# Performance work log

Hardware: AMD Instinct MI355X
Metric: run time of the kernel (lower is better)

## Reference

```python
import jax, jax.numpy as jnp
import numpy as np

B, S, H, D = 2, 2048, 16, 128
HID = H * D
THETA = 10000.0
SCALE = 1.0 / np.sqrt(D)


def setup_inputs() -> dict:
    key = jax.random.key(0)
    k1, k2, k3 = jax.random.split(key, 3)
    x = jax.random.normal(k1, (B, S, HID), dtype=jnp.float32)
    w_qkv = jax.random.normal(k2, (3 * HID, HID), dtype=jnp.float32) * 0.02
    w_o = jax.random.normal(k3, (HID, HID), dtype=jnp.float32) * 0.02
    return {"x": x, "w_qkv": w_qkv, "w_o": w_o}


def _rope_cos_sin(seq_len, dim, dtype):
    inv_freq = 1.0 / (THETA ** (jnp.arange(0, dim, 2, dtype=jnp.float32) / dim))
    pos = jnp.arange(seq_len, dtype=jnp.float32)
    freqs = pos[:, None] * inv_freq[None, :]          # (S, D/2)
    emb = jnp.concatenate([freqs, freqs], axis=-1)    # (S, D)
    return jnp.cos(emb).astype(dtype), jnp.sin(emb).astype(dtype)


def _rotate_half(t):
    t1, t2 = jnp.split(t, 2, axis=-1)
    return jnp.concatenate([-t2, t1], axis=-1)


def reference(x, w_qkv, w_o):
    b, s, _ = x.shape
    qkv = jnp.einsum('bsh,oh->bso', x, w_qkv)                 # (B,S,3*HID)
    qkv = qkv.reshape(b, s, 3, H, D).transpose(2, 0, 3, 1, 4)  # (3,B,H,S,D)
    q, k, v = qkv[0], qkv[1], qkv[2]
    cos, sin = _rope_cos_sin(s, D, x.dtype)                    # (S,D)
    q = q * cos + _rotate_half(q) * sin
    k = k * cos + _rotate_half(k) * sin
    scores = jnp.einsum('bhqd,bhkd->bhqk', q, k) * SCALE       # (B,H,S,S)
    causal = jnp.triu(jnp.ones((s, s), dtype=bool), k=1)
    scores = jnp.where(causal[None, None], -jnp.inf, scores)
    attn = jax.nn.softmax(scores.astype(jnp.float32), axis=-1).astype(q.dtype)
    out = jnp.einsum('bhqk,bhkd->bhqd', attn, v)               # (B,H,S,D)
    out = out.transpose(0, 2, 1, 3).reshape(b, s, HID)
    return jnp.einsum('bsh,oh->bso', out, w_o)
```

## Files before the change

### kernel.cpp

```cpp
#include <hip/hip_runtime.h>
#include <hip/hip_bf16.h>

typedef unsigned short u16;
typedef unsigned long long u64;
typedef u16 us8 __attribute__((ext_vector_type(8)));
typedef __bf16 bf8_t __attribute__((ext_vector_type(8)));
typedef float f32x4 __attribute__((ext_vector_type(4)));

__device__ __forceinline__ float b2f(u16 u) {
    return __uint_as_float(((unsigned int)u) << 16);
}
__device__ __forceinline__ u16 f2b(float f) {
    union { __hip_bfloat16 h; u16 u; } v;
    v.h = __float2bfloat16(f);
    return v.u;
}
__device__ __forceinline__ f32x4 mfma16(bf8_t a, bf8_t b, f32x4 c) {
    return __builtin_amdgcn_mfma_f32_16x16x32_bf16(a, b, c, 0, 0, 0);
}
__device__ __forceinline__ void gload_lds16(const u16* g, u16* lds_base) {
    __builtin_amdgcn_global_load_lds((const __attribute__((address_space(1))) unsigned int*)g,
                                     (__attribute__((address_space(3))) unsigned int*)lds_base,
                                     16, 0, 0);
}

__global__ __launch_bounds__(256) void f32_to_bf16(const float* __restrict__ src,
                                                   u16* __restrict__ dst, int n8) {
    int idx = blockIdx.x * 256 + threadIdx.x;
    if (idx >= n8) return;
    float4 f0 = ((const float4*)src)[idx * 2];
    float4 f1 = ((const float4*)src)[idx * 2 + 1];
    us8 o;
    o[0] = f2b(f0.x); o[1] = f2b(f0.y); o[2] = f2b(f0.z); o[3] = f2b(f0.w);
    o[4] = f2b(f1.x); o[5] = f2b(f1.y); o[6] = f2b(f1.z); o[7] = f2b(f1.w);
    ((us8*)dst)[idx] = o;
}

#define BARX() __builtin_amdgcn_s_barrier()
#define LGKM0() do { asm volatile("s_waitcnt lgkmcnt(0)" ::: "memory"); \
                     __builtin_amdgcn_sched_barrier(0); } while (0)
#define VMN() do { \
    if constexpr (AH == 2) asm volatile("s_waitcnt vmcnt(4)" ::: "memory"); \
    else                   asm volatile("s_waitcnt vmcnt(2)" ::: "memory"); \
    __builtin_amdgcn_sched_barrier(0); } while (0)

template<int SF32, int AH>
__global__ __launch_bounds__(512, 2) void gemm256(const u16* __restrict__ A,
                                                  const u16* __restrict__ B,
                                                  void* __restrict__ Cout, int ldc) {
    constexpr int MF = AH * 4;
    constexpr int MH = AH * 2;

    __shared__ u16 LA[2][AH * 128 * 64];
    __shared__ u16 LB[2][256 * 64];

    const int tid = threadIdx.x;
    const int w = tid >> 6, lane = tid & 63;
    const int lm = lane & 15, lq = lane >> 4;
    const int wm = w >> 2, wn = w & 3;

    const int bid = blockIdx.x;
    const int nper = gridDim.x >> 3;
    const int wg = (bid & 7) * nper + (bid >> 3);
    const int mt = (AH == 2) ? (wg & 15) : (wg & 31);
    const int nt = (AH == 2) ? (wg >> 4) : (wg >> 5);
    const int m0 = mt * (AH * 128), n0 = nt * 256;

    const int srow = lane >> 3;
    const int scol = ((lane & 7) ^ srow) * 8;

    const u16* Ag = A + (size_t)(m0 + srow) * 2048 + scol;
    const u16* Bg = B + (size_t)(n0 + srow) * 2048 + scol;

#define STAGE_A(c, h, kt) do { \
    _Pragma("unroll") \
    for (int i = 0; i < 2; i++) { \
        int R = w * 2 + i; \
        gload_lds16(Ag + (size_t)((h) * 128 + R * 8) * 2048 + (kt) * 64, \
                    &LA[c][((h) * 128 + R * 8) * 64]); \
    } } while (0)

#define STAGE_B(c, h, kt) do { \
    _Pragma("unroll") \
    for (int i = 0; i < 2; i++) { \
        int R = w * 2 + i; \
        gload_lds16(Bg + (size_t)((h) * 128 + R * 8) * 2048 + (kt) * 64, \
                    &LB[c][((h) * 128 + R * 8) * 64]); \
    } } while (0)

    bf8_t af[MF][2], bfr[4][2];
    f32x4 acc[MF][4] = {};
    const int cswz = (lm & 7) << 4;

#define RD_A(c, mh) do { \
    _Pragma("unroll") \
    for (int m = 0; m < MH; m++) \
    _Pragma("unroll") \
    for (int ks = 0; ks < 2; ks++) { \
        int row = wm * (AH * 64) + ((mh) * MH + m) * 16 + lm; \
        int o = (row * 128 + ks * 64 + lq * 16) ^ cswz; \
        af[(mh) * MH + m][ks] = *(const bf8_t*)((const char*)&LA[c][0] + o); \
    } } while (0)

#define RD_B(c, nh) do { \
    _Pragma("unroll") \
    for (int n = 0; n < 2; n++) \
    _Pragma("unroll") \
    for (int ks = 0; ks < 2; ks++) { \
        int row = wn * 64 + ((nh) * 2 + n) * 16 + lm; \
        int o = (row * 128 + ks * 64 + lq * 16) ^ cswz; \
        bfr[(nh) * 2 + n][ks] = *(const bf8_t*)((const char*)&LB[c][0] + o); \
    } } while (0)

#define QUAD(mh, nh) do { \
    __builtin_amdgcn_s_setprio(1); \
    _Pragma("unroll") \
    for (int m = 0; m < MH; m++) \
    _Pragma("unroll") \
    for (int n = 0; n < 2; n++) \
    _Pragma("unroll") \
    for (int ks = 0; ks < 2; ks++) \
        acc[(mh) * MH + m][(nh) * 2 + n] = mfma16(af[(mh) * MH + m][ks], \
            bfr[(nh) * 2 + n][ks], acc[(mh) * MH + m][(nh) * 2 + n]); \
    __builtin_amdgcn_s_setprio(0); \
    } while (0)

#define TILE(c, tB, tA) do { \
    RD_A(c, 0); RD_B(c, 0); \
    STAGE_B((c) ^ 1, 0, tB); \
    BARX(); LGKM0(); \
    QUAD(0, 0); \
    BARX(); \
    RD_A(c, 1); \
    STAGE_B((c) ^ 1, 1, tB); \
    BARX(); LGKM0(); \
    QUAD(1, 0); \
    BARX(); \
    RD_B(c, 1); \
    STAGE_A(c, 0, tA); \
    BARX(); LGKM0(); \
    QUAD(0, 1); \
    BARX(); \
    if constexpr (AH == 2) STAGE_A(c, 1, tA); \
    QUAD(1, 1); \
    VMN(); \
    BARX(); \
} while (0)

    STAGE_A(0, 0, 0);
    if constexpr (AH == 2) STAGE_A(0, 1, 0);
    STAGE_B(0, 0, 0); STAGE_B(0, 1, 0);
    STAGE_A(1, 0, 1);
    if constexpr (AH == 2) STAGE_A(1, 1, 1);
    VMN();
    BARX();

    for (int it = 0; it < 16; it++) {
        const int t0 = 2 * it, t1 = 2 * it + 1;
        const int tB0 = t1;
        const int tA0 = (t0 + 2 < 32) ? t0 + 2 : 31;
        const int tB1 = (t1 + 1 < 32) ? t1 + 1 : 31;
        const int tA1 = (t1 + 2 < 32) ? t1 + 2 : 31;
        TILE(0, tB0, tA0);
        TILE(1, tB1, tA1);
    }

#pragma unroll
    for (int m = 0; m < MF; m++)
#pragma unroll
        for (int n = 0; n < 4; n++)
#pragma unroll
            for (int r = 0; r < 4; r++) {
                int row = m0 + wm * (AH * 64) + m * 16 + lq * 4 + r;
                int col = n0 + wn * 64 + n * 16 + lm;
                if (SF32)
                    ((float*)Cout)[(size_t)row * ldc + col] = acc[m][n][r];
                else
                    ((u16*)Cout)[(size_t)row * ldc + col] = f2b(acc[m][n][r]);
            }
#undef TILE
#undef QUAD
#undef RD_A
#undef RD_B
#undef STAGE_A
#undef STAGE_B
}

__global__ __launch_bounds__(256) void rope_vt(u16* __restrict__ qkv, u16* __restrict__ VT) {
    __shared__ u16 T[64 * 136];
    const int tid = threadIdx.x;
    const int s0 = blockIdx.x * 64;
    const int bh = blockIdx.y;
    const int b = bh >> 4, h = bh & 15;
#pragma unroll
    for (int p = 0; p < 4; p++) {
        int sl = p * 16 + (tid >> 4);
        int d0 = (tid & 15) * 8;
        *(us8*)&T[sl * 136 + d0] =
            *(const us8*)(qkv + ((size_t)(b * 2048 + s0 + sl)) * 6144 + 4096 + h * 128 + d0);
    }
#pragma unroll
    for (int p = 0; p < 2; p++) {
        int task = p * 256 + tid;
        int sl = task >> 3;
        int jg = task & 7;
        size_t base = ((size_t)(b * 2048 + s0 + sl)) * 6144 + h * 128 + jg * 8;
        us8 qlo = *(const us8*)(qkv + base);
        us8 qhi = *(const us8*)(qkv + base + 64);
        us8 klo = *(const us8*)(qkv + base + 2048);
        us8 khi = *(const us8*)(qkv + base + 2048 + 64);
        us8 oql, oqh, okl, okh;
        float s = (float)(s0 + sl);
#pragma unroll
        for (int e = 0; e < 8; e++) {
            int j = jg * 8 + e;
            float inv = __expf((float)j * (-9.210340371976184f / 64.f));
            float ang = s * inv;
            float sn, c;
            __sincosf(ang, &sn, &c);
            float q1 = b2f(qlo[e]), q2 = b2f(qhi[e]);
            oql[e] = f2b(q1 * c - q2 * sn);
            oqh[e] = f2b(q2 * c + q1 * sn);
            float k1 = b2f(klo[e]), k2 = b2f(khi[e]);
            okl[e] = f2b(k1 * c - k2 * sn);
            okh[e] = f2b(k2 * c + k1 * sn);
        }
        *(us8*)(qkv + base) = oql;
        *(us8*)(qkv + base + 64) = oqh;
        *(us8*)(qkv + base + 2048) = okl;
        *(us8*)(qkv + base + 2048 + 64) = okh;
    }
    __syncthreads();
#pragma unroll
    for (int p = 0; p < 4; p++) {
        int idx = p * 256 + tid;
        int d = idx & 127;
        int sg = idx >> 7;
        us8 v;
#pragma unroll
        for (int i = 0; i < 8; i++) v[i] = T[(sg * 8 + i) * 136 + d];
        *(us8*)&VT[((size_t)bh * 128 + d) * 2048 + s0 + sg * 8] = v;
    }
}

#define ATT_SCALE 0.08838834764831845f

__global__ __launch_bounds__(256, 2) void attn_flash(const u16* __restrict__ qkv, const u16* __restrict__ VT,
                                                     u16* __restrict__ AO) {
    const int bid = blockIdx.x;
    const int swz = (bid & 7) * 64 + (bid >> 3);
    const int bh = swz >> 4;
    const int pair = swz & 15;
    const int b = bh >> 4, h = bh & 15;
    const int tid = threadIdx.x, lane = tid & 63, wave = tid >> 6;
    const int lm = lane & 15, lq = lane >> 4;

    const int jq0 = 31 - pair;
    const int jq1 = pair;
    const int ktmax = jq0;

    __shared__ u16 Kt[64 * 136];
    __shared__ u16 Vt[128 * 72];

    bf8_t qf[2][4];
#pragma unroll
    for (int qg = 0; qg < 2; qg++) {
        const int jqv = qg ? jq1 : jq0;
        const u16* Qrow = qkv + ((size_t)(b * 2048 + jqv * 64 + wave * 16 + lm)) * 6144 + h * 128;
#pragma unroll
        for (int ks = 0; ks < 4; ks++)
            qf[qg][ks] = *(const bf8_t*)(Qrow + ks * 32 + lq * 8);
    }

    f32x4 Of[2][8] = {};
    float mrun[2] = {-3.0e38f, -3.0e38f}, lrun[2] = {0.f, 0.f};

    const u16* Kbase = qkv + (size_t)b * 2048 * 6144 + 2048 + h * 128;
    const u16* VTbase = VT + (size_t)bh * 128 * 2048;

    const int krow = tid >> 4;
    const int kcol = (tid & 15) * 8;
    const int vrow = tid >> 3;
    const int vcol = (tid & 7) * 8;

    us8 kreg[4], vreg[4];
#pragma unroll
    for (int p = 0; p < 4; p++) {
        kreg[p] = *(const us8*)(Kbase + (size_t)(p * 16 + krow) * 6144 + kcol);
        vreg[p] = *(const us8*)(VTbase + (size_t)(p * 32 + vrow) * 2048 + vcol);
    }

    for (int kt = 0; kt <= ktmax; kt++) {
        __syncthreads();
#pragma unroll
        for (int p = 0; p < 4; p++) {
            *(us8*)&Kt[(p * 16 + krow) * 136 + kcol] = kreg[p];
            *(us8*)&Vt[(p * 32 + vrow) * 72 + vcol] = vreg[p];
        }
        __syncthreads();
        {
            int kn = (kt + 1 <= ktmax ? kt + 1 : ktmax) * 64;
#pragma unroll
            for (int p = 0; p < 4; p++) {
                kreg[p] = *(const us8*)(Kbase + (size_t)(kn + p * 16 + krow) * 6144 + kcol);
                vreg[p] = *(const us8*)(VTbase + (size_t)(p * 32 + vrow) * 2048 + kn + vcol);
            }
        }

        const bool act1 = (kt <= jq1);
        u64 pk[2][4];
#pragma unroll
        for (int qg = 0; qg < 2; qg++) {
            if (qg == 0 || act1) {
                const int jqv = qg ? jq1 : jq0;
                float sv[4][4];
#pragma unroll
                for (int nb = 0; nb < 4; nb++) {
                    f32x4 a = {};
#pragma unroll
                    for (int ks = 0; ks < 4; ks++) {
                        bf8_t kf = *(const bf8_t*)&Kt[(nb * 16 + lm) * 136 + ks * 32 + lq * 8];
                        a = mfma16(kf, qf[qg][ks], a);
                    }
#pragma unroll
                    for (int r = 0; r < 4; r++) sv[nb][r] = a[r] * ATT_SCALE;
                }
                if (kt == jqv) {
                    int qglob = jqv * 64 + wave * 16 + lm;
#pragma unroll
                    for (int nb = 0; nb < 4; nb++)
#pragma unroll
                        for (int r = 0; r < 4; r++)
                            if (kt * 64 + nb * 16 + lq * 4 + r > qglob) sv[nb][r] = -3.0e38f;
                }
                float mx = -3.0e38f;
#pragma unroll
                for (int nb = 0; nb < 4; nb++)
#pragma unroll
                    for (int r = 0; r < 4; r++) mx = fmaxf(mx, sv[nb][r]);
                mx = fmaxf(mx, __shfl_xor(mx, 16, 64));
                mx = fmaxf(mx, __shfl_xor(mx, 32, 64));
                float mnew = fmaxf(mrun[qg], mx);
                float a_ = __expf(mrun[qg] - mnew);
                float rs = 0.f;
#pragma unroll
                for (int nb = 0; nb < 4; nb++) {
                    float e0 = __expf(sv[nb][0] - mnew), e1 = __expf(sv[nb][1] - mnew);
                    float e2 = __expf(sv[nb][2] - mnew), e3 = __expf(sv[nb][3] - mnew);
                    rs += (e0 + e1) + (e2 + e3);
                    unsigned int lo = (unsigned int)f2b(e0) | ((unsigned int)f2b(e1) << 16);
                    unsigned int hi = (unsigned int)f2b(e2) | ((unsigned int)f2b(e3) << 16);
                    pk[qg][nb] = (u64)lo | ((u64)hi << 32);
                }
                rs += __shfl_xor(rs, 16, 64);
                rs += __shfl_xor(rs, 32, 64);
                lrun[qg] = lrun[qg] * a_ + rs;
                mrun[qg] = mnew;
#pragma unroll
                for (int db = 0; db < 8; db++)
#pragma unroll
                    for (int r = 0; r < 4; r++) Of[qg][db][r] *= a_;
            }
        }

        const int slo = ((lq & 1) * 2) * 16 + lm;
        const int shi = slo + 16;
        const bool sel = (lq >> 1) != 0;
#pragma unroll
        for (int kk = 0; kk < 2; kk++) {
            union { u64 v[2]; bf8_t f; } pf[2];
#pragma unroll
            for (int qg = 0; qg < 2; qg++) {
                if (qg == 0 || act1) {
                    u64 lo0 = __shfl(pk[qg][2 * kk + 0], slo, 64);
                    u64 lo1 = __shfl(pk[qg][2 * kk + 1], slo, 64);
                    u64 hi0 = __shfl(pk[qg][2 * kk + 0], shi, 64);
                    u64 hi1 = __shfl(pk[qg][2 * kk + 1], shi, 64);
                    pf[qg].v[0] = sel ? lo1 : lo0;
                    pf[qg].v[1] = sel ? hi1 : hi0;
                }
            }
#pragma unroll
            for (int db = 0; db < 8; db++) {
                bf8_t vf = *(const bf8_t*)&Vt[(db * 16 + lm) * 72 + kk * 32 + lq * 8];
                Of[0][db] = mfma16(vf, pf[0].f, Of[0][db]);
                if (act1) Of[1][db] = mfma16(vf, pf[1].f, Of[1][db]);
            }
        }
    }
#pragma unroll
    for (int qg = 0; qg < 2; qg++) {
        const int jqv = qg ? jq1 : jq0;
        float invl = 1.f / lrun[qg];
        size_t rowbase = (size_t)(b * 2048 + jqv * 64 + wave * 16 + lm) * 2048 + h * 128;
#pragma unroll
        for (int db = 0; db < 8; db++) {
            ushort4 o;
            o.x = f2b(Of[qg][db][0] * invl);
            o.y = f2b(Of[qg][db][1] * invl);
            o.z = f2b(Of[qg][db][2] * invl);
            o.w = f2b(Of[qg][db][3] * invl);
            *(ushort4*)(AO + rowbase + db * 16 + lq * 4) = o;
        }
    }
}

extern "C" void kernel_launch(void* const* d_in, const int* in_sizes, int n_in,
                              void* d_out, int out_size, void* d_ws, size_t ws_size,
                              hipStream_t stream) {
    const float* x     = (const float*)d_in[0];
    const float* w_qkv = (const float*)d_in[1];
    const float* w_o   = (const float*)d_in[2];
    float* out = (float*)d_out;
    u16* ws = (u16*)d_ws;

    u16* qkvb  = ws;
    u16* VT    = ws + 25165824;
    u16* AO    = ws + 33554432;
    u16* xb    = ws + 41943040;
    u16* wqkvb = ws + 50331648;
    u16* wob   = ws + 62914560;

    f32_to_bf16<<<4096, 256, 0, stream>>>(x, xb, 1048576);
    f32_to_bf16<<<6144, 256, 0, stream>>>(w_qkv, wqkvb, 1572864);
    f32_to_bf16<<<2048, 256, 0, stream>>>(w_o, wob, 524288);
    gemm256<0, 2><<<384, 512, 0, stream>>>(xb, wqkvb, qkvb, 6144);
    rope_vt<<<dim3(32, 32), 256, 0, stream>>>(qkvb, VT);
    attn_flash<<<dim3(512), 256, 0, stream>>>(qkvb, VT, AO);
    gemm256<1, 1><<<256, 512, 0, stream>>>(AO, wob, out, 2048);
}
```

Measured before the change: 416.1 us.

## Retile QKV GEMM to 256x192 blocks for a single full wave

Replaces the 256x256 QKV projection GEMM with a 256x192 tile kernel so the grid has 512 blocks, matching two blocks per CU across the device instead of a partial second wave. The warp layout and the LDS staging and pipelining schedule are reworked for the new tile shape. The output projection GEMM is split into its own specialized kernel with unchanged logic. The narrower tile lowers per-block reuse and changes the wait-count pipelining, which could expose load latency.

```diff
diff --git a/kernel.cpp b/kernel.cpp
--- a/kernel.cpp
+++ b/kernel.cpp
@@ -39,32 +39,25 @@
 #define BARX() __builtin_amdgcn_s_barrier()
 #define LGKM0() do { asm volatile("s_waitcnt lgkmcnt(0)" ::: "memory"); \
                      __builtin_amdgcn_sched_barrier(0); } while (0)
-#define VMN() do { \
-    if constexpr (AH == 2) asm volatile("s_waitcnt vmcnt(4)" ::: "memory"); \
-    else                   asm volatile("s_waitcnt vmcnt(2)" ::: "memory"); \
-    __builtin_amdgcn_sched_barrier(0); } while (0)
-
-template<int SF32, int AH>
-__global__ __launch_bounds__(512, 2) void gemm256(const u16* __restrict__ A,
+#define VM4A()  do { asm volatile("s_waitcnt vmcnt(4)" ::: "memory"); \
+                     __builtin_amdgcn_sched_barrier(0); } while (0)
+
+__global__ __launch_bounds__(512, 2) void gemm192(const u16* __restrict__ A,
                                                   const u16* __restrict__ B,
-                                                  void* __restrict__ Cout, int ldc) {
-    constexpr int MF = AH * 4;
-    constexpr int MH = AH * 2;
-
-    __shared__ u16 LA[2][AH * 128 * 64];
-    __shared__ u16 LB[2][256 * 64];
+                                                  u16* __restrict__ Cout, int ldc) {
+    __shared__ u16 LA[2][256 * 64];
+    __shared__ u16 LB[2][192 * 64];
 
     const int tid = threadIdx.x;
     const int w = tid >> 6, lane = tid & 63;
     const int lm = lane & 15, lq = lane >> 4;
-    const int wm = w >> 2, wn = w & 3;
+    const int wm = w >> 1, wn = w & 1;
 
     const int bid = blockIdx.x;
     const int nper = gridDim.x >> 3;
     const int wg = (bid & 7) * nper + (bid >> 3);
-    const int mt = (AH == 2) ? (wg & 15) : (wg & 31);
-    const int nt = (AH == 2) ? (wg >> 4) : (wg >> 5);
-    const int m0 = mt * (AH * 128), n0 = nt * 256;
+    const int mt = wg & 15, nt = wg >> 4;
+    const int m0 = mt * 256, n0 = nt * 192;
 
     const int srow = lane >> 3;
     const int scol = ((lane & 7) ^ srow) * 8;
@@ -72,87 +65,80 @@
     const u16* Ag = A + (size_t)(m0 + srow) * 2048 + scol;
     const u16* Bg = B + (size_t)(n0 + srow) * 2048 + scol;
 
-#define STAGE_A(c, h, kt) do { \
-    _Pragma("unroll") \
-    for (int i = 0; i < 2; i++) { \
-        int R = w * 2 + i; \
-        gload_lds16(Ag + (size_t)((h) * 128 + R * 8) * 2048 + (kt) * 64, \
-                    &LA[c][((h) * 128 + R * 8) * 64]); \
-    } } while (0)
-
-#define STAGE_B(c, h, kt) do { \
-    _Pragma("unroll") \
-    for (int i = 0; i < 2; i++) { \
-        int R = w * 2 + i; \
-        gload_lds16(Bg + (size_t)((h) * 128 + R * 8) * 2048 + (kt) * 64, \
-                    &LB[c][((h) * 128 + R * 8) * 64]); \
-    } } while (0)
-
-    bf8_t af[MF][2], bfr[4][2];
-    f32x4 acc[MF][4] = {};
+#define STAGE_A2(c, kt, jb) do { \
+    _Pragma("unroll") \
+    for (int j = 0; j < 2; j++) { \
+        int R = ((jb) + j) * 64 + w * 8; \
+        gload_lds16(Ag + (size_t)R * 2048 + (kt) * 64, &LA[c][R * 64]); \
+    } } while (0)
+
+#define STAGE_B3(c, kt) do { \
+    _Pragma("unroll") \
+    for (int j = 0; j < 3; j++) { \
+        int R = j * 64 + w * 8; \
+        gload_lds16(Bg + (size_t)R * 2048 + (kt) * 64, &LB[c][R * 64]); \
+    } } while (0)
+
+    bf8_t af[4][2], bfr[6][2];
+    f32x4 acc[4][6] = {};
     const int cswz = (lm & 7) << 4;
 
-#define RD_A(c, mh) do { \
-    _Pragma("unroll") \
-    for (int m = 0; m < MH; m++) \
+#define RD_A4(c) do { \
+    _Pragma("unroll") \
+    for (int m = 0; m < 4; m++) \
     _Pragma("unroll") \
     for (int ks = 0; ks < 2; ks++) { \
-        int row = wm * (AH * 64) + ((mh) * MH + m) * 16 + lm; \
+        int row = wm * 64 + m * 16 + lm; \
         int o = (row * 128 + ks * 64 + lq * 16) ^ cswz; \
-        af[(mh) * MH + m][ks] = *(const bf8_t*)((const char*)&LA[c][0] + o); \
-    } } while (0)
-
-#define RD_B(c, nh) do { \
+        af[m][ks] = *(const bf8_t*)((const char*)&LA[c][0] + o); \
+    } } while (0)
+
+#define RD_B2(c, np) do { \
     _Pragma("unroll") \
     for (int n = 0; n < 2; n++) \
     _Pragma("unroll") \
     for (int ks = 0; ks < 2; ks++) { \
-        int row = wn * 64 + ((nh) * 2 + n) * 16 + lm; \
+        int row = wn * 96 + ((np) * 2 + n) * 16 + lm; \
         int o = (row * 128 + ks * 64 + lq * 16) ^ cswz; \
-        bfr[(nh) * 2 + n][ks] = *(const bf8_t*)((const char*)&LB[c][0] + o); \
-    } } while (0)
-
-#define QUAD(mh, nh) do { \
+        bfr[(np) * 2 + n][ks] = *(const bf8_t*)((const char*)&LB[c][0] + o); \
+    } } while (0)
+
+#define QUAD6(np) do { \
     __builtin_amdgcn_s_setprio(1); \
     _Pragma("unroll") \
-    for (int m = 0; m < MH; m++) \
+    for (int m = 0; m < 4; m++) \
     _Pragma("unroll") \
     for (int n = 0; n < 2; n++) \
     _Pragma("unroll") \
     for (int ks = 0; ks < 2; ks++) \
-        acc[(mh) * MH + m][(nh) * 2 + n] = mfma16(af[(mh) * MH + m][ks], \
-            bfr[(nh) * 2 + n][ks], acc[(mh) * MH + m][(nh) * 2 + n]); \
+        acc[m][(np) * 2 + n] = mfma16(af[m][ks], bfr[(np) * 2 + n][ks], \
+                                      acc[m][(np) * 2 + n]); \
     __builtin_amdgcn_s_setprio(0); \
     } while (0)
 
-#define TILE(c, tB, tA) do { \
-    RD_A(c, 0); RD_B(c, 0); \
-    STAGE_B((c) ^ 1, 0, tB); \
+#define TILE192(c, tB, tA) do { \
+    RD_A4(c); RD_B2(c, 0); \
+    STAGE_B3((c) ^ 1, tB); \
     BARX(); LGKM0(); \
-    QUAD(0, 0); \
-    BARX(); \
-    RD_A(c, 1); \
-    STAGE_B((c) ^ 1, 1, tB); \
+    QUAD6(0); \
+    BARX(); \
+    RD_B2(c, 1); \
+    STAGE_A2(c, tA, 0); \
     BARX(); LGKM0(); \
-    QUAD(1, 0); \
-    BARX(); \
-    RD_B(c, 1); \
-    STAGE_A(c, 0, tA); \
+    QUAD6(1); \
+    BARX(); \
+    RD_B2(c, 2); \
+    STAGE_A2(c, tA, 2); \
     BARX(); LGKM0(); \
-    QUAD(0, 1); \
-    BARX(); \
-    if constexpr (AH == 2) STAGE_A(c, 1, tA); \
-    QUAD(1, 1); \
-    VMN(); \
+    QUAD6(2); \
+    VM4A(); \
     BARX(); \
 } while (0)
 
-    STAGE_A(0, 0, 0);
-    if constexpr (AH == 2) STAGE_A(0, 1, 0);
-    STAGE_B(0, 0, 0); STAGE_B(0, 1, 0);
-    STAGE_A(1, 0, 1);
-    if constexpr (AH == 2) STAGE_A(1, 1, 1);
-    VMN();
+    STAGE_A2(0, 0, 0); STAGE_A2(0, 0, 2);
+    STAGE_B3(0, 0);
+    STAGE_A2(1, 1, 0); STAGE_A2(1, 1, 2);
+    VM4A();
     BARX();
 
     for (int it = 0; it < 16; it++) {
@@ -161,24 +147,156 @@
         const int tA0 = (t0 + 2 < 32) ? t0 + 2 : 31;
         const int tB1 = (t1 + 1 < 32) ? t1 + 1 : 31;
         const int tA1 = (t1 + 2 < 32) ? t1 + 2 : 31;
-        TILE(0, tB0, tA0);
-        TILE(1, tB1, tA1);
-    }
-
-#pragma unroll
-    for (int m = 0; m < MF; m++)
+        TILE192(0, tB0, tA0);
+        TILE192(1, tB1, tA1);
+    }
+
+#pragma unroll
+    for (int m = 0; m < 4; m++)
+#pragma unroll
+        for (int n = 0; n < 6; n++)
+#pragma unroll
+            for (int r = 0; r < 4; r++) {
+                int row = m0 + wm * 64 + m * 16 + lq * 4 + r;
+                int col = n0 + wn * 96 + n * 16 + lm;
+                Cout[(size_t)row * ldc + col] = f2b(acc[m][n][r]);
+            }
+#undef TILE192
+#undef QUAD6
+#undef RD_A4
+#undef RD_B2
+#undef STAGE_A2
+#undef STAGE_B3
+}
+
+#define VMN() do { \
+    asm volatile("s_waitcnt vmcnt(2)" ::: "memory"); \
+    __builtin_amdgcn_sched_barrier(0); } while (0)
+
+__global__ __launch_bounds__(512, 2) void gemm_op(const u16* __restrict__ A,
+                                                  const u16* __restrict__ B,
+                                                  float* __restrict__ Cout, int ldc) {
+    __shared__ u16 LA[2][128 * 64];
+    __shared__ u16 LB[2][256 * 64];
+
+    const int tid = threadIdx.x;
+    const int w = tid >> 6, lane = tid & 63;
+    const int lm = lane & 15, lq = lane >> 4;
+    const int wm = w >> 2, wn = w & 3;
+
+    const int bid = blockIdx.x;
+    const int nper = gridDim.x >> 3;
+    const int wg = (bid & 7) * nper + (bid >> 3);
+    const int mt = wg & 31, nt = wg >> 5;
+    const int m0 = mt * 128, n0 = nt * 256;
+
+    const int srow = lane >> 3;
+    const int scol = ((lane & 7) ^ srow) * 8;
+
+    const u16* Ag = A + (size_t)(m0 + srow) * 2048 + scol;
+    const u16* Bg = B + (size_t)(n0 + srow) * 2048 + scol;
+
+#define STAGE_A(c, h, kt) do { \
+    _Pragma("unroll") \
+    for (int i = 0; i < 2; i++) { \
+        int R = w * 2 + i; \
+        if ((h) == 0) \
+            gload_lds16(Ag + (size_t)(R * 8) * 2048 + (kt) * 64, &LA[c][(R * 8) * 64]); \
+    } } while (0)
+
+#define STAGE_B(c, h, kt) do { \
+    _Pragma("unroll") \
+    for (int i = 0; i < 2; i++) { \
+        int R = w * 2 + i; \
+        gload_lds16(Bg + (size_t)((h) * 128 + R * 8) * 2048 + (kt) * 64, \
+                    &LB[c][((h) * 128 + R * 8) * 64]); \
+    } } while (0)
+
+    bf8_t af[4][2], bfr[4][2];
+    f32x4 acc[4][4] = {};
+    const int cswz = (lm & 7) << 4;
+
+#define RD_A(c, mh) do { \
+    _Pragma("unroll") \
+    for (int m = 0; m < 2; m++) \
+    _Pragma("unroll") \
+    for (int ks = 0; ks < 2; ks++) { \
+        int row = wm * 64 + ((mh) * 2 + m) * 16 + lm; \
+        int o = (row * 128 + ks * 64 + lq * 16) ^ cswz; \
+        af[(mh) * 2 + m][ks] = *(const bf8_t*)((const char*)&LA[c][0] + o); \
+    } } while (0)
+
+#define RD_B(c, nh) do { \
+    _Pragma("unroll") \
+    for (int n = 0; n < 2; n++) \
+    _Pragma("unroll") \
+    for (int ks = 0; ks < 2; ks++) { \
+        int row = wn * 64 + ((nh) * 2 + n) * 16 + lm; \
+        int o = (row * 128 + ks * 64 + lq * 16) ^ cswz; \
+        bfr[(nh) * 2 + n][ks] = *(const bf8_t*)((const char*)&LB[c][0] + o); \
+    } } while (0)
+
+#define QUAD(mh, nh) do { \
+    __builtin_amdgcn_s_setprio(1); \
+    _Pragma("unroll") \
+    for (int m = 0; m < 2; m++) \
+    _Pragma("unroll") \
+    for (int n = 0; n < 2; n++) \
+    _Pragma("unroll") \
+    for (int ks = 0; ks < 2; ks++) \
+        acc[(mh) * 2 + m][(nh) * 2 + n] = mfma16(af[(mh) * 2 + m][ks], \
+            bfr[(nh) * 2 + n][ks], acc[(mh) * 2 + m][(nh) * 2 + n]); \
+    __builtin_amdgcn_s_setprio(0); \
+    } while (0)
+
+#define TILEOP(c, tB, tA) do { \
+    RD_A(c, 0); RD_B(c, 0); \
+    STAGE_B((c) ^ 1, 0, tB); \
+    BARX(); LGKM0(); \
+    QUAD(0, 0); \
+    BARX(); \
+    RD_A(c, 1); \
+    STAGE_B((c) ^ 1, 1, tB); \
+    BARX(); LGKM0(); \
+    QUAD(1, 0); \
+    BARX(); \
+    RD_B(c, 1); \
+    STAGE_A(c, 0, tA); \
+    BARX(); LGKM0(); \
+    QUAD(0, 1); \
+    BARX(); \
+    QUAD(1, 1); \
+    VMN(); \
+    BARX(); \
+} while (0)
+
+    STAGE_A(0, 0, 0);
+    STAGE_B(0, 0, 0); STAGE_B(0, 1, 0);
+    STAGE_A(1, 0, 1);
+    VMN();
+    BARX();
+
+    for (int it = 0; it < 16; it++) {
+        const int t0 = 2 * it, t1 = 2 * it + 1;
+        const int tB0 = t1;
+        const int tA0 = (t0 + 2 < 32) ? t0 + 2 : 31;
+        const int tB1 = (t1 + 1 < 32) ? t1 + 1 : 31;
+        const int tA1 = (t1 + 2 < 32) ? t1 + 2 : 31;
+        TILEOP(0, tB0, tA0);
+        TILEOP(1, tB1, tA1);
+    }
+
+#pragma unroll
+    for (int m = 0; m < 4; m++)
 #pragma unroll
         for (int n = 0; n < 4; n++)
 #pragma unroll
             for (int r = 0; r < 4; r++) {
-                int row = m0 + wm * (AH * 64) + m * 16 + lq * 4 + r;
+                int row = m0 + wm * 64 + m * 16 + lq * 4 + r;
                 int col = n0 + wn * 64 + n * 16 + lm;
-                if (SF32)
-                    ((float*)Cout)[(size_t)row * ldc + col] = acc[m][n][r];
-                else
-                    ((u16*)Cout)[(size_t)row * ldc + col] = f2b(acc[m][n][r]);
+                Cout[(size_t)row * ldc + col] = acc[m][n][r];
             }
-#undef TILE
+#undef TILEOP
 #undef QUAD
 #undef RD_A
 #undef RD_B
@@ -424,8 +542,8 @@
     f32_to_bf16<<<4096, 256, 0, stream>>>(x, xb, 1048576);
     f32_to_bf16<<<6144, 256, 0, stream>>>(w_qkv, wqkvb, 1572864);
     f32_to_bf16<<<2048, 256, 0, stream>>>(w_o, wob, 524288);
-    gemm256<0, 2><<<384, 512, 0, stream>>>(xb, wqkvb, qkvb, 6144);
+    gemm192<<<512, 512, 0, stream>>>(xb, wqkvb, qkvb, 6144);
     rope_vt<<<dim3(32, 32), 256, 0, stream>>>(qkvb, VT);
     attn_flash<<<dim3(512), 256, 0, stream>>>(qkvb, VT, AO);
-    gemm256<1, 1><<<256, 512, 0, stream>>>(AO, wob, out, 2048);
-}
+    gemm_op<<<256, 512, 0, stream>>>(AO, wob, out, 2048);
+}
```

Measured after the change: 380.6 us. 1.09x faster.
